# Performance work log

Hardware: AMD Instinct MI355X
Metric: run time of the kernel (lower is better)

## Reference

```python
import jax, jax.numpy as jnp
import numpy as np

B, S, D = 16, 2048, 64
SCALE = 1.0 / np.sqrt(np.float32(D))  # forward divides by sqrt(embedding_dim=64)


def setup_inputs() -> dict:
    key = jax.random.key(0)
    ks = jax.random.split(key, 7)
    return {
        "x": jax.random.normal(ks[0], (B, S, D), dtype=jnp.float32),
        "Wq": jax.random.normal(ks[1], (D, D), dtype=jnp.float32) * 0.02,
        "bq": jax.random.normal(ks[2], (D,), dtype=jnp.float32) * 0.02,
        "Wk": jax.random.normal(ks[3], (D, D), dtype=jnp.float32) * 0.02,
        "bk": jax.random.normal(ks[4], (D,), dtype=jnp.float32) * 0.02,
        "Wv": jax.random.normal(ks[5], (D, D), dtype=jnp.float32) * 0.02,
        "bv": jax.random.normal(ks[6], (D,), dtype=jnp.float32) * 0.02,
    }


def reference(x, Wq, bq, Wk, bk, Wv, bv):
    # Linear projections (weights stored [in, out], math-equivalent to nn.Linear)
    q = jnp.einsum("bsd,de->bse", x, Wq) + bq
    k = jnp.einsum("bsd,de->bse", x, Wk) + bk
    v = jnp.einsum("bsd,de->bse", x, Wv) + bv
    # Unfused scores: [B, S, S]
    scores = jnp.einsum("bqd,bkd->bqk", q, k) * jnp.float32(SCALE)
    causal = jnp.tril(jnp.ones((S, S), dtype=bool))  # mask[:S,:S]
    scores = jnp.where(causal, scores, jnp.float32(-jnp.inf))
    attn = jax.nn.softmax(scores, axis=-1)
    # dropout is identity in eval mode (reference baseline)
    out = jnp.einsum("bqk,bkd->bqd", attn, v)
    return out
```

## Files before the change

kernel.cpp:

```cpp
#include <hip/hip_runtime.h>

#define NB 16
#define SS 2048
#define DD 64

typedef __attribute__((ext_vector_type(8))) short short8;
typedef __attribute__((ext_vector_type(4))) float f32x4;

#define SCL2E 0.18033688011112042f

__device__ __forceinline__ short f2bf(float f) {
  union { float f; unsigned u; } v; v.f = f;
  unsigned r = (v.u + 0x7fffu + ((v.u >> 16) & 1u)) >> 16;
  return (short)r;
}

__device__ __forceinline__ short8 load_a_frag_f32(const float* p) {
  float4 u = *(const float4*)p;
  float4 w = *(const float4*)(p + 4);
  short8 r;
  r[0] = f2bf(u.x); r[1] = f2bf(u.y); r[2] = f2bf(u.z); r[3] = f2bf(u.w);
  r[4] = f2bf(w.x); r[5] = f2bf(w.y); r[6] = f2bf(w.z); r[7] = f2bf(w.w);
  return r;
}

__global__ __launch_bounds__(256) void proj_kernel(
    const float* __restrict__ x,
    const float* __restrict__ Wq, const float* __restrict__ bq,
    const float* __restrict__ Wk, const float* __restrict__ bk,
    const float* __restrict__ Wv, const float* __restrict__ bv,
    ushort* __restrict__ qo, ushort* __restrict__ ko, ushort* __restrict__ vT)
{
  __shared__ __align__(16) ushort Wt[3][64][72];
  __shared__ __align__(16) ushort Vs[64][68];
  const int t = threadIdx.x;
  {
    const float* Ws[3] = {Wq, Wk, Wv};
    for (int m = 0; m < 3; ++m)
      for (int i = 0; i < 4; ++i) {
        int idx = i * 1024 + t * 4;
        int kk = idx >> 6, n0 = idx & 63;
        float4 w4 = *(const float4*)(Ws[m] + kk * 64 + n0);
        Wt[m][n0 + 0][kk] = (ushort)f2bf(w4.x);
        Wt[m][n0 + 1][kk] = (ushort)f2bf(w4.y);
        Wt[m][n0 + 2][kk] = (ushort)f2bf(w4.z);
        Wt[m][n0 + 3][kk] = (ushort)f2bf(w4.w);
      }
  }
  __syncthreads();

  const int lane = t & 63, w = t >> 6;
  const int l15 = lane & 15, quad = lane >> 4;
  const int g = blockIdx.x * 64 + w * 16 + l15;
  short8 a0 = load_a_frag_f32(x + (size_t)g * 64 + quad * 8);
  short8 a1 = load_a_frag_f32(x + (size_t)g * 64 + 32 + quad * 8);
  const int lrow0 = w * 16 + quad * 4;
  const int row0 = blockIdx.x * 64 + lrow0;

  for (int m = 0; m < 3; ++m) {
    const float* bp = (m == 0 ? bq : (m == 1 ? bk : bv));
    for (int nt = 0; nt < 4; ++nt) {
      short8 b0 = *(const short8*)&Wt[m][nt * 16 + l15][quad * 8];
      short8 b1 = *(const short8*)&Wt[m][nt * 16 + l15][32 + quad * 8];
      f32x4 acc = {0.f, 0.f, 0.f, 0.f};
      acc = __builtin_amdgcn_mfma_f32_16x16x32_bf16(a0, b0, acc, 0, 0, 0);
      acc = __builtin_amdgcn_mfma_f32_16x16x32_bf16(a1, b1, acc, 0, 0, 0);
      float bb = bp[nt * 16 + l15];
      if (m == 0) {
        for (int r = 0; r < 4; ++r)
          qo[(size_t)(row0 + r) * 64 + nt * 16 + l15] = (ushort)f2bf(acc[r] + bb);
      } else if (m == 1) {
        for (int r = 0; r < 4; ++r)
          ko[(size_t)(row0 + r) * 64 + nt * 16 + l15] = (ushort)f2bf(acc[r] + bb);
      } else {
        for (int r = 0; r < 4; ++r)
          Vs[lrow0 + r][nt * 16 + l15] = (ushort)f2bf(acc[r] + bb);
      }
    }
  }
  __syncthreads();
  {
    const int batch = blockIdx.x >> 5;
    const int s0 = (blockIdx.x & 31) * 64;
    const int d = t >> 2, j0 = (t & 3) * 16;
    ushort tmp[16];
    for (int j = 0; j < 16; ++j) tmp[j] = Vs[j0 + j][d];
    ushort* dst = vT + (size_t)batch * DD * SS + (size_t)d * SS + s0 + j0;
    ((int4*)dst)[0] = ((int4*)tmp)[0];
    ((int4*)dst)[1] = ((int4*)tmp)[1];
  }
}

template<bool MASKED>
__device__ __forceinline__ void attn_half(
    const f32x4 (&c)[4], float (&l_part)[4], f32x4 (&acc)[4],
    const short8 (&vf0)[4], const short8 (&vf1)[4],
    ushort* __restrict__ Pw, int keyb, int rowb, int l15, int quad)
{
#pragma unroll
  for (int ct = 0; ct < 4; ++ct)
#pragma unroll
    for (int r = 0; r < 4; ++r) {
      float pe = __builtin_amdgcn_exp2f(c[ct][r] * SCL2E);
      if (MASKED && (keyb + ct * 16 > rowb + r)) pe = 0.f;
      l_part[r] += pe;
      Pw[(quad * 4 + r) * 72 + ct * 16 + l15] = (ushort)f2bf(pe);
    }
  short8 pa0 = *(const short8*)&Pw[l15 * 72 + quad * 8];
  short8 pa1 = *(const short8*)&Pw[l15 * 72 + 32 + quad * 8];
#pragma unroll
  for (int nt = 0; nt < 4; ++nt) {
    acc[nt] = __builtin_amdgcn_mfma_f32_16x16x32_bf16(pa0, vf0[nt], acc[nt], 0, 0, 0);
    acc[nt] = __builtin_amdgcn_mfma_f32_16x16x32_bf16(pa1, vf1[nt], acc[nt], 0, 0, 0);
  }
}

__global__ __launch_bounds__(256, 3) void attn_kernel(
    const ushort* __restrict__ qg, const ushort* __restrict__ kg,
    const ushort* __restrict__ vT, float* __restrict__ out)
{
  __shared__ __align__(16) float accW[4][32][68];
  __shared__ float lW[4][32];
  ushort* Pw_base = (ushort*)&accW[0][0][0];

  const int t = threadIdx.x, bid = blockIdx.x;
  const int batch = (bid & 7) * 2 + ((bid >> 3) & 1);
  const int qt = 63 - (bid >> 4);
  const int q0 = qt * 32;
  const int lane = t & 63, w = t >> 6;
  const int l15 = lane & 15, quad = lane >> 4;
  const size_t bbase = (size_t)batch * SS * DD;
  ushort* Pw = Pw_base + w * (16 * 72);

  const ushort* qp = qg + bbase + (size_t)(q0 + l15) * 64 + quad * 8;
  short8 a0 = *(const short8*)qp;
  short8 a1 = *(const short8*)(qp + 32);
  short8 a2 = *(const short8*)(qp + 16 * 64);
  short8 a3 = *(const short8*)(qp + 16 * 64 + 32);

  f32x4 acc0[4], acc1[4];
  float l0[4] = {0.f, 0.f, 0.f, 0.f}, l1[4] = {0.f, 0.f, 0.f, 0.f};
#pragma unroll
  for (int nt = 0; nt < 4; ++nt) {
    acc0[nt] = (f32x4){0.f, 0.f, 0.f, 0.f};
    acc1[nt] = (f32x4){0.f, 0.f, 0.f, 0.f};
  }

  const int ktotal = ((q0 + 31) >> 6) + 1;
  const ushort* kp0 = kg + bbase + (size_t)(w * 64 + l15) * 64 + quad * 8;
  const ushort* kp1 = kp0 + 2048;
  const ushort* vp0 = vT + bbase + (size_t)(l15) * SS + w * 64 + quad * 8;
  const ushort* vp1 = vp0 + 16 * SS;
  const ushort* vp2 = vp0 + 32 * SS;
  const ushort* vp3 = vp0 + 48 * SS;

  for (int kt = w; kt < ktotal; kt += 4) {
    short8 kf0[4], kf1[4], vf0[4], vf1[4];
    kf0[0] = *(const short8*)(kp0);
    kf1[0] = *(const short8*)(kp0 + 32);
    kf0[1] = *(const short8*)(kp0 + 1024);
    kf1[1] = *(const short8*)(kp0 + 1056);
    kf0[2] = *(const short8*)(kp1);
    kf1[2] = *(const short8*)(kp1 + 32);
    kf0[3] = *(const short8*)(kp1 + 1024);
    kf1[3] = *(const short8*)(kp1 + 1056);
    vf0[0] = *(const short8*)(vp0); vf1[0] = *(const short8*)(vp0 + 32);
    vf0[1] = *(const short8*)(vp1); vf1[1] = *(const short8*)(vp1 + 32);
    vf0[2] = *(const short8*)(vp2); vf1[2] = *(const short8*)(vp2 + 32);
    vf0[3] = *(const short8*)(vp3); vf1[3] = *(const short8*)(vp3 + 32);

    f32x4 c0[4], c1[4];
#pragma unroll
    for (int ct = 0; ct < 4; ++ct) {
      c0[ct] = (f32x4){0.f, 0.f, 0.f, 0.f};
      c0[ct] = __builtin_amdgcn_mfma_f32_16x16x32_bf16(a0, kf0[ct], c0[ct], 0, 0, 0);
      c0[ct] = __builtin_amdgcn_mfma_f32_16x16x32_bf16(a1, kf1[ct], c0[ct], 0, 0, 0);
      c1[ct] = (f32x4){0.f, 0.f, 0.f, 0.f};
      c1[ct] = __builtin_amdgcn_mfma_f32_16x16x32_bf16(a2, kf0[ct], c1[ct], 0, 0, 0);
      c1[ct] = __builtin_amdgcn_mfma_f32_16x16x32_bf16(a3, kf1[ct], c1[ct], 0, 0, 0);
    }

    const int kb = kt * 64;
    if (kt == ktotal - 1) {
      attn_half<true >(c0, l0, acc0, vf0, vf1, Pw, kb + l15, q0 + quad * 4, l15, quad);
      attn_half<true >(c1, l1, acc1, vf0, vf1, Pw, kb + l15, q0 + 16 + quad * 4, l15, quad);
    } else {
      attn_half<false>(c0, l0, acc0, vf0, vf1, Pw, kb + l15, q0 + quad * 4, l15, quad);
      attn_half<false>(c1, l1, acc1, vf0, vf1, Pw, kb + l15, q0 + 16 + quad * 4, l15, quad);
    }
    kp0 += 16384; kp1 += 16384;
    vp0 += 256; vp1 += 256; vp2 += 256; vp3 += 256;
  }

#pragma unroll
  for (int r = 0; r < 4; ++r)
    for (int off = 1; off < 16; off <<= 1) {
      l0[r] += __shfl_xor(l0[r], off, 64);
      l1[r] += __shfl_xor(l1[r], off, 64);
    }

  __syncthreads();
#pragma unroll
  for (int r = 0; r < 4; ++r)
#pragma unroll
    for (int nt = 0; nt < 4; ++nt) {
      accW[w][quad * 4 + r][nt * 16 + l15] = acc0[nt][r];
      accW[w][16 + quad * 4 + r][nt * 16 + l15] = acc1[nt][r];
    }
  if (l15 == 0)
#pragma unroll
    for (int r = 0; r < 4; ++r) {
      lW[w][quad * 4 + r] = l0[r];
      lW[w][16 + quad * 4 + r] = l1[r];
    }
  __syncthreads();

  {
    const int row = t >> 3, col0 = (t & 7) * 8;
    float den = lW[0][row] + lW[1][row] + lW[2][row] + lW[3][row];
    float iv = 1.0f / den;
    float4 oa = {0.f, 0.f, 0.f, 0.f}, ob = {0.f, 0.f, 0.f, 0.f};
#pragma unroll
    for (int ww = 0; ww < 4; ++ww) {
      float4 x0 = *(const float4*)&accW[ww][row][col0];
      float4 x1 = *(const float4*)&accW[ww][row][col0 + 4];
      oa.x += x0.x; oa.y += x0.y; oa.z += x0.z; oa.w += x0.w;
      ob.x += x1.x; ob.y += x1.y; ob.z += x1.z; ob.w += x1.w;
    }
    oa.x *= iv; oa.y *= iv; oa.z *= iv; oa.w *= iv;
    ob.x *= iv; ob.y *= iv; ob.z *= iv; ob.w *= iv;
    float* op = out + bbase + (size_t)(q0 + row) * 64 + col0;
    *(float4*)op = oa;
    *(float4*)(op + 4) = ob;
  }
}

extern "C" void kernel_launch(void* const* d_in, const int* in_sizes, int n_in,
                              void* d_out, int out_size, void* d_ws, size_t ws_size,
                              hipStream_t stream) {
  (void)in_sizes; (void)n_in; (void)out_size; (void)ws_size;
  const float* x  = (const float*)d_in[0];
  const float* Wq = (const float*)d_in[1];
  const float* bq = (const float*)d_in[2];
  const float* Wk = (const float*)d_in[3];
  const float* bk = (const float*)d_in[4];
  const float* Wv = (const float*)d_in[5];
  const float* bv = (const float*)d_in[6];
  float* out = (float*)d_out;

  ushort* qws = (ushort*)d_ws;
  ushort* kws = qws + (size_t)NB * SS * DD;
  ushort* vws = kws + (size_t)NB * SS * DD;

  proj_kernel<<<dim3(NB * SS / 64), dim3(256), 0, stream>>>(
      x, Wq, bq, Wk, bk, Wv, bv, qws, kws, vws);
  attn_kernel<<<dim3(NB * (SS / 32)), dim3(256), 0, stream>>>(
      qws, kws, vws, out);
}
```

Baseline: 116.5 us.

## Prefetch next K tile into registers and permute key columns for vector P stores

```diff
diff --git a/kernel.cpp b/kernel.cpp
--- a/kernel.cpp
+++ b/kernel.cpp
@@ -1,4 +1,5 @@
 #include <hip/hip_runtime.h>
+#include <hip/hip_bf16.h>
 
 #define NB 16
 #define SS 2048
@@ -95,17 +96,24 @@
 __device__ __forceinline__ void attn_half(
     const f32x4 (&c)[4], float (&l_part)[4], f32x4 (&acc)[4],
     const short8 (&vf0)[4], const short8 (&vf1)[4],
-    ushort* __restrict__ Pw, int keyb, int rowb, int l15, int quad)
+    ushort* __restrict__ Pw, int kb4, int rowb, int l15, int quad)
 {
 #pragma unroll
-  for (int ct = 0; ct < 4; ++ct)
-#pragma unroll
-    for (int r = 0; r < 4; ++r) {
-      float pe = __builtin_amdgcn_exp2f(c[ct][r] * SCL2E);
-      if (MASKED && (keyb + ct * 16 > rowb + r)) pe = 0.f;
-      l_part[r] += pe;
-      Pw[(quad * 4 + r) * 72 + ct * 16 + l15] = (ushort)f2bf(pe);
-    }
+  for (int r = 0; r < 4; ++r) {
+    float pe[4];
+#pragma unroll
+    for (int ct = 0; ct < 4; ++ct) {
+      pe[ct] = __builtin_amdgcn_exp2f(c[ct][r] * SCL2E);
+      if (MASKED && (kb4 + ct > rowb + r)) pe[ct] = 0.f;
+    }
+    l_part[r] += (pe[0] + pe[1]) + (pe[2] + pe[3]);
+    __hip_bfloat162 h01 = __float22bfloat162_rn(make_float2(pe[0], pe[1]));
+    __hip_bfloat162 h23 = __float22bfloat162_rn(make_float2(pe[2], pe[3]));
+    uint2 pwv;
+    pwv.x = *reinterpret_cast<unsigned*>(&h01);
+    pwv.y = *reinterpret_cast<unsigned*>(&h23);
+    *(uint2*)&Pw[(quad * 4 + r) * 72 + 4 * l15] = pwv;
+  }
   short8 pa0 = *(const short8*)&Pw[l15 * 72 + quad * 8];
   short8 pa1 = *(const short8*)&Pw[l15 * 72 + 32 + quad * 8];
 #pragma unroll
@@ -115,7 +123,7 @@
   }
 }
 
-__global__ __launch_bounds__(256, 3) void attn_kernel(
+__global__ __launch_bounds__(256, 2) void attn_kernel(
     const ushort* __restrict__ qg, const ushort* __restrict__ kg,
     const ushort* __restrict__ vT, float* __restrict__ out)
 {
@@ -147,48 +155,58 @@
   }
 
   const int ktotal = ((q0 + 31) >> 6) + 1;
-  const ushort* kp0 = kg + bbase + (size_t)(w * 64 + l15) * 64 + quad * 8;
-  const ushort* kp1 = kp0 + 2048;
-  const ushort* vp0 = vT + bbase + (size_t)(l15) * SS + w * 64 + quad * 8;
+  const ushort* kpc = kg + bbase + (size_t)(4 * l15) * 64 + quad * 8
+                    + (size_t)(w << 6) * 64;
+  const ushort* vp0 = vT + bbase + (size_t)l15 * SS + w * 64 + quad * 8;
   const ushort* vp1 = vp0 + 16 * SS;
   const ushort* vp2 = vp0 + 32 * SS;
   const ushort* vp3 = vp0 + 48 * SS;
 
+  short8 kc0[4], kc1[4];
+#pragma unroll
+  for (int ct = 0; ct < 4; ++ct) {
+    kc0[ct] = *(const short8*)(kpc + ct * 64);
+    kc1[ct] = *(const short8*)(kpc + ct * 64 + 32);
+  }
+
   for (int kt = w; kt < ktotal; kt += 4) {
-    short8 kf0[4], kf1[4], vf0[4], vf1[4];
-    kf0[0] = *(const short8*)(kp0);
-    kf1[0] = *(const short8*)(kp0 + 32);
-    kf0[1] = *(const short8*)(kp0 + 1024);
-    kf1[1] = *(const short8*)(kp0 + 1056);
-    kf0[2] = *(const short8*)(kp1);
-    kf1[2] = *(const short8*)(kp1 + 32);
-    kf0[3] = *(const short8*)(kp1 + 1024);
-    kf1[3] = *(const short8*)(kp1 + 1056);
+    short8 vf0[4], vf1[4];
     vf0[0] = *(const short8*)(vp0); vf1[0] = *(const short8*)(vp0 + 32);
     vf0[1] = *(const short8*)(vp1); vf1[1] = *(const short8*)(vp1 + 32);
     vf0[2] = *(const short8*)(vp2); vf1[2] = *(const short8*)(vp2 + 32);
     vf0[3] = *(const short8*)(vp3); vf1[3] = *(const short8*)(vp3 + 32);
 
+    const ushort* kpn = (kt + 4 < ktotal) ? (kpc + 16384) : kpc;
+    short8 kn0[4], kn1[4];
+#pragma unroll
+    for (int ct = 0; ct < 4; ++ct) {
+      kn0[ct] = *(const short8*)(kpn + ct * 64);
+      kn1[ct] = *(const short8*)(kpn + ct * 64 + 32);
+    }
+
     f32x4 c0[4], c1[4];
 #pragma unroll
     for (int ct = 0; ct < 4; ++ct) {
       c0[ct] = (f32x4){0.f, 0.f, 0.f, 0.f};
-      c0[ct] = __builtin_amdgcn_mfma_f32_16x16x32_bf16(a0, kf0[ct], c0[ct], 0, 0, 0);
-      c0[ct] = __builtin_amdgcn_mfma_f32_16x16x32_bf16(a1, kf1[ct], c0[ct], 0, 0, 0);
+      c0[ct] = __builtin_amdgcn_mfma_f32_16x16x32_bf16(a0, kc0[ct], c0[ct], 0, 0, 0);
+      c0[ct] = __builtin_amdgcn_mfma_f32_16x16x32_bf16(a1, kc1[ct], c0[ct], 0, 0, 0);
       c1[ct] = (f32x4){0.f, 0.f, 0.f, 0.f};
-      c1[ct] = __builtin_amdgcn_mfma_f32_16x16x32_bf16(a2, kf0[ct], c1[ct], 0, 0, 0);
-      c1[ct] = __builtin_amdgcn_mfma_f32_16x16x32_bf16(a3, kf1[ct], c1[ct], 0, 0, 0);
-    }
-
-    const int kb = kt * 64;
+      c1[ct] = __builtin_amdgcn_mfma_f32_16x16x32_bf16(a2, kc0[ct], c1[ct], 0, 0, 0);
+      c1[ct] = __builtin_amdgcn_mfma_f32_16x16x32_bf16(a3, kc1[ct], c1[ct], 0, 0, 0);
+    }
+
+    const int kb4 = kt * 64 + 4 * l15;
     if (kt == ktotal - 1) {
-      attn_half<true >(c0, l0, acc0, vf0, vf1, Pw, kb + l15, q0 + quad * 4, l15, quad);
-      attn_half<true >(c1, l1, acc1, vf0, vf1, Pw, kb + l15, q0 + 16 + quad * 4, l15, quad);
+      attn_half<true >(c0, l0, acc0, vf0, vf1, Pw, kb4, q0 + quad * 4, l15, quad);
+      attn_half<true >(c1, l1, acc1, vf0, vf1, Pw, kb4, q0 + 16 + quad * 4, l15, quad);
     } else {
-      attn_half<false>(c0, l0, acc0, vf0, vf1, Pw, kb + l15, q0 + quad * 4, l15, quad);
-      attn_half<false>(c1, l1, acc1, vf0, vf1, Pw, kb + l15, q0 + 16 + quad * 4, l15, quad);
-    }
-    kp0 += 16384; kp1 += 16384;
+      attn_half<false>(c0, l0, acc0, vf0, vf1, Pw, kb4, q0 + quad * 4, l15, quad);
+      attn_half<false>(c1, l1, acc1, vf0, vf1, Pw, kb4, q0 + 16 + quad * 4, l15, quad);
+    }
+
+#pragma unroll
+    for (int ct = 0; ct < 4; ++ct) { kc0[ct] = kn0[ct]; kc1[ct] = kn1[ct]; }
+    kpc = kpn;
     vp0 += 256; vp1 += 256; vp2 += 256; vp3 += 256;
   }
 
```

Result: no change. 118.6 us (+1.8%).
